# Kernel tuning notes

Measured on AMD Instinct MI355X. Metric: run time of the kernel, lower is better.

Reference implementation:

```python
import jax, jax.numpy as jnp
import numpy as np

N_NODES, N_EDGES = 16384, 8192
IN_CH, HID_CH = 256, 256
ALPHA, BETA = -1.5, -0.5


def setup_inputs() -> dict:
    key = jax.random.key(0)
    k1, k2, k3, k4, k5, k6 = jax.random.split(key, 6)
    x_0 = jax.random.normal(k1, (N_NODES, IN_CH), dtype=jnp.float32)
    # binary incidence matrix (n_nodes, n_edges)
    incidence_1 = jax.random.randint(k2, (N_NODES, N_EDGES), 0, 2).astype(jnp.float32)
    # conv weights (torch Conv: x @ W then neighborhood @ .)
    W0 = jax.random.normal(k3, (IN_CH, HID_CH), dtype=jnp.float32) * 0.02
    W1 = jax.random.normal(k4, (HID_CH, HID_CH), dtype=jnp.float32) * 0.02
    # xavier_uniform biases of shape (1, hidden)
    gain = 1.414
    bound = gain * np.sqrt(6.0 / (1 + HID_CH)) * np.sqrt(3.0) / np.sqrt(3.0)  # xavier bound = gain*sqrt(6/(fan_in+fan_out))
    bound = gain * np.sqrt(6.0 / (1 + HID_CH))
    bias_0_to_1 = jax.random.uniform(k5, (1, HID_CH), minval=-bound, maxval=bound, dtype=jnp.float32)
    bias_1_to_0 = jax.random.uniform(k6, (1, HID_CH), minval=-bound, maxval=bound, dtype=jnp.float32)
    return {"x_0": x_0, "incidence_1": incidence_1, "W0": W0, "W1": W1,
            "bias_0_to_1": bias_0_to_1, "bias_1_to_0": bias_1_to_0}


def _normalize_incidence(B1):
    # edge/node cardinalities raised to alpha/beta
    edge_card = jnp.sum(B1, axis=0) ** ALPHA          # (n_edges,)
    node_card = jnp.sum(B1, axis=1) ** BETA           # (n_nodes,)
    mask = (B1 > 0).astype(B1.dtype)
    d0_inv = 1.0 / (mask @ edge_card)                 # (n_nodes,) per-node sum of incident edge_card
    d1_inv = 1.0 / (mask.T @ node_card)               # (n_edges,) per-edge sum of member node_card
    # B1_norm = D0_left^-1 @ B1 @ diag(edge_card)
    B1_norm = d0_inv[:, None] * B1 * edge_card[None, :]
    # B1T_norm = D1_left^-1 @ B1^T @ diag(node_card)
    B1T_norm = d1_inv[:, None] * B1.T * node_card[None, :]
    return B1_norm, B1T_norm


def reference(x_0, incidence_1, W0, W1, bias_0_to_1, bias_1_to_0):
    B1_norm, B1T_norm = _normalize_incidence(incidence_1)
    # node -> edge conv: x_1 = B1T_norm @ (x_0 @ W0) + b01
    x_1 = B1T_norm @ (x_0 @ W0) + bias_0_to_1        # (n_edges, hid)
    # edge -> node conv: x_0 = B1_norm @ (x_1 @ W1) + b10
    x_0_out = B1_norm @ (x_1 @ W1) + bias_1_to_0     # (n_nodes, hid)
    return jax.nn.relu(x_0_out), jax.nn.relu(x_1)
```

## Files before the change

kernel.cpp:

```cpp
#include <hip/hip_runtime.h>
#include <stdint.h>

#define NN 16384
#define NE 8192
#define CH 256
#define MM1_SPLIT 8
#define MM2_SPLIT 4

typedef __attribute__((ext_vector_type(8))) short bf16x8;
typedef __attribute__((ext_vector_type(4))) float f32x4;

__device__ __forceinline__ unsigned short f2bf(float f) {
  unsigned u = __float_as_uint(f);
  u += 0x7FFFu + ((u >> 16) & 1u);
  return (unsigned short)(u >> 16);
}
__device__ __forceinline__ void async_copy16(const void* gptr, void* lptr) {
  __builtin_amdgcn_global_load_lds((const __attribute__((address_space(1))) unsigned int*)gptr,
                                   (__attribute__((address_space(3))) unsigned int*)lptr,
                                   16, 0, 0);
}

__device__ __forceinline__ void transpose32(unsigned* x) {
  const unsigned masks[5] = {0x0000FFFFu, 0x00FF00FFu, 0x0F0F0F0Fu, 0x33333333u, 0x55555555u};
#pragma unroll
  for (int jj = 0; jj < 5; ++jj) {
    const int j = 16 >> jj;
    const unsigned m = masks[jj];
#pragma unroll
    for (int k = 0; k < 32; ++k) {
      if ((k & j) == 0) {
        unsigned t = ((x[k] >> j) ^ x[k + j]) & m;
        x[k] ^= (t << j);
        x[k + j] ^= t;
      }
    }
  }
}

__global__ void k0_transpose_w(const float* __restrict__ W0, const float* __restrict__ W1,
                               unsigned short* __restrict__ W0T, unsigned short* __restrict__ W1T) {
  const float* W = blockIdx.y ? W1 : W0;
  unsigned short* WT = blockIdx.y ? W1T : W0T;
  int n = blockIdx.x;
  int k = threadIdx.x;
  WT[n * CH + k] = f2bf(W[k * CH + n]);
}

__global__ void k1_pack_card(const float* __restrict__ B1, unsigned* __restrict__ pk1,
                             float* __restrict__ node_card) {
  int n = blockIdx.x;
  int t = threadIdx.x;
  const float4* p = (const float4*)(B1 + (size_t)n * NE + t * 32);
  unsigned w = 0;
#pragma unroll
  for (int jj = 0; jj < 8; ++jj) {
    float4 v = p[jj];
    w |= ((__float_as_uint(v.x) >> 23) & 1u) << (4 * jj);
    w |= ((__float_as_uint(v.y) >> 23) & 1u) << (4 * jj + 1);
    w |= ((__float_as_uint(v.z) >> 23) & 1u) << (4 * jj + 2);
    w |= ((__float_as_uint(v.w) >> 23) & 1u) << (4 * jj + 3);
  }
  pk1[(size_t)n * 256 + t] = w;
  int s = __popc(w);
  __shared__ int red[4];
#pragma unroll
  for (int off = 32; off; off >>= 1) s += __shfl_down(s, off, 64);
  if ((t & 63) == 0) red[t >> 6] = s;
  __syncthreads();
  if (t == 0) {
    float tot = (float)(red[0] + red[1] + red[2] + red[3]);
    node_card[n] = rsqrtf(tot);
  }
}

__global__ __launch_bounds__(256) void k1b_bitT(const unsigned* __restrict__ pk1,
                                                unsigned* __restrict__ pk1T) {
  int bw = blockIdx.x & 127;
  int half = blockIdx.x >> 7;
  int t = threadIdx.x;
  int nt = half * 256 + t;
  unsigned x0[32], x1[32];
#pragma unroll
  for (int r = 0; r < 32; ++r) {
    uint2 v = *(const uint2*)&pk1[(size_t)(nt * 32 + r) * 256 + 2 * bw];
    x0[r] = v.x;
    x1[r] = v.y;
  }
  transpose32(x0);
  transpose32(x1);
  int e0 = bw * 64;
#pragma unroll
  for (int c = 0; c < 32; ++c) {
    pk1T[(size_t)(e0 + c) * 512 + nt] = x0[c];
    pk1T[(size_t)(e0 + 32 + c) * 512 + nt] = x1[c];
  }
}

__global__ __launch_bounds__(256) void k2_y0(const float* __restrict__ X0,
                                             const unsigned short* __restrict__ W0T,
                                             const float* __restrict__ node_card,
                                             unsigned short* __restrict__ y0sT) {
  __shared__ __align__(16) unsigned short a_lds[64 * 32];
  __shared__ __align__(16) unsigned short b_lds[256 * 32];
  const int tid = threadIdx.x;
  const int wave = tid >> 6, lane = tid & 63;
  const int quad = lane >> 4, l15 = lane & 15;
  const int m0 = blockIdx.x * 64;
  const int ar = tid >> 3, ac = (tid & 7) * 4;

  f32x4 acc[4][4];
  const f32x4 fz = {0.f, 0.f, 0.f, 0.f};
#pragma unroll
  for (int i = 0; i < 4; ++i)
#pragma unroll
    for (int j = 0; j < 4; ++j) acc[i][j] = fz;

  for (int k0 = 0; k0 < CH; k0 += 32) {
    __syncthreads();
#pragma unroll
    for (int p = 0; p < 2; ++p) {
      float4 v = *(const float4*)(X0 + (size_t)(m0 + ar + p * 32) * CH + k0 + ac);
      uint2 w;
      w.x = ((unsigned)f2bf(v.x)) | ((unsigned)f2bf(v.y) << 16);
      w.y = ((unsigned)f2bf(v.z)) | ((unsigned)f2bf(v.w) << 16);
      *(uint2*)&a_lds[(ar + p * 32) * 32 + ac] = w;
    }
#pragma unroll
    for (int i = 0; i < 4; ++i) {
      int rowbase = wave * 64 + i * 16;
      const unsigned short* g = W0T + (size_t)(rowbase + (lane >> 2)) * CH + k0 + (lane & 3) * 8;
      async_copy16(g, &b_lds[rowbase * 32]);
    }
    __syncthreads();
    bf16x8 af[4];
#pragma unroll
    for (int i = 0; i < 4; ++i)
      af[i] = *(const bf16x8*)&a_lds[(i * 16 + l15) * 32 + quad * 8];
#pragma unroll
    for (int j = 0; j < 4; ++j) {
      bf16x8 bfr = *(const bf16x8*)&b_lds[(wave * 64 + j * 16 + l15) * 32 + quad * 8];
#pragma unroll
      for (int i = 0; i < 4; ++i)
        acc[i][j] = __builtin_amdgcn_mfma_f32_16x16x32_bf16(af[i], bfr, acc[i][j], 0, 0, 0);
    }
  }
#pragma unroll
  for (int i = 0; i < 4; ++i) {
    int row4 = m0 + i * 16 + quad * 4;
    float4 nc = *(const float4*)(node_card + row4);
#pragma unroll
    for (int j = 0; j < 4; ++j) {
      int col = wave * 64 + j * 16 + l15;
      f32x4 v = acc[i][j];
      ushort4 o;
      o.x = f2bf(v[0] * nc.x);
      o.y = f2bf(v[1] * nc.y);
      o.z = f2bf(v[2] * nc.z);
      o.w = f2bf(v[3] * nc.w);
      *(ushort4*)&y0sT[(size_t)col * NN + row4] = o;
    }
  }
}

__global__ void k2b_aux(const float* __restrict__ node_card, unsigned short* __restrict__ y0sT) {
  int n = blockIdx.x * 256 + threadIdx.x;
  y0sT[(size_t)256 * NN + n] = f2bf(node_card[n]);
  y0sT[(size_t)257 * NN + n] = 0x3F80;
#pragma unroll
  for (int r = 258; r < 272; ++r) y0sT[(size_t)r * NN + n] = 0;
}

__global__ __launch_bounds__(256) void mm1_kernel(const unsigned char* __restrict__ pk1T,
                                                  const unsigned short* __restrict__ y0sT,
                                                  float* __restrict__ mm1p,
                                                  float* __restrict__ auxD,
                                                  float* __restrict__ auxC) {
  __shared__ __align__(16) unsigned short a_lds[64 * 40];
  __shared__ __align__(16) unsigned short b_lds[272 * 32];
  const int tid = threadIdx.x;
  const int wave = tid >> 6, lane = tid & 63;
  const int quad = lane >> 4, l15 = lane & 15;
  const int m0 = blockIdx.x * 64;
  const int sp = blockIdx.y;
  const int KS = NN / MM1_SPLIT;
  const int kbase = sp * KS;

  const int am = tid >> 2;
  const int akg = tid & 3;
  const int ajbs = akg ^ ((am >> 4) & 3);
  unsigned short* aw_dst = &a_lds[am * 40 + ajbs * 8];

  f32x4 acc[4][4];
  f32x4 acc5[4];
  const f32x4 fz = {0.f, 0.f, 0.f, 0.f};
#pragma unroll
  for (int i = 0; i < 4; ++i) {
    acc5[i] = fz;
#pragma unroll
    for (int j = 0; j < 4; ++j) acc[i][j] = fz;
  }

  const unsigned char* agp = pk1T + (size_t)(m0 + am) * (NN / 8) + (kbase >> 3) + akg;
  unsigned abyte = *agp;

  for (int kk = 0; kk < KS; kk += 32) {
    const int k0 = kbase + kk;
    __syncthreads();
    {
      uint4 aw;
#pragma unroll
      for (int j = 0; j < 4; ++j) {
        unsigned lo = (abyte >> (2 * j)) & 1u;
        unsigned hi = (abyte >> (2 * j + 1)) & 1u;
        ((unsigned*)&aw)[j] = lo * 0x3F80u + hi * 0x3F800000u;
      }
      *(uint4*)aw_dst = aw;
    }
#pragma unroll
    for (int i = 0; i < 4; ++i) {
      int rowbase = wave * 64 + i * 16;
      const unsigned short* g = y0sT + (size_t)(rowbase + (lane >> 2)) * NN + k0 + (lane & 3) * 8;
      async_copy16(g, &b_lds[rowbase * 32]);
    }
    if (wave == 3) {
      const unsigned short* g = y0sT + (size_t)(256 + (lane >> 2)) * NN + k0 + (lane & 3) * 8;
      async_copy16(g, &b_lds[256 * 32]);
    }
    __syncthreads();
    if (kk + 32 < KS) {
      agp += 4;
      abyte = *agp;
    }
    bf16x8 af[4];
#pragma unroll
    for (int i = 0; i < 4; ++i) {
      int m = i * 16 + l15;
      int jbs = quad ^ ((m >> 4) & 3);
      af[i] = *(const bf16x8*)&a_lds[m * 40 + jbs * 8];
    }
#pragma unroll
    for (int j = 0; j < 4; ++j) {
      bf16x8 bfr = *(const bf16x8*)&b_lds[(wave * 64 + j * 16 + l15) * 32 + quad * 8];
#pragma unroll
      for (int i = 0; i < 4; ++i)
        acc[i][j] = __builtin_amdgcn_mfma_f32_16x16x32_bf16(af[i], bfr, acc[i][j], 0, 0, 0);
    }
    if (wave == 3) {
      bf16x8 bfr = *(const bf16x8*)&b_lds[(256 + l15) * 32 + quad * 8];
#pragma unroll
      for (int i = 0; i < 4; ++i)
        acc5[i] = __builtin_amdgcn_mfma_f32_16x16x32_bf16(af[i], bfr, acc5[i], 0, 0, 0);
    }
  }
  float* outp = mm1p + (size_t)sp * NE * CH;
#pragma unroll
  for (int i = 0; i < 4; ++i) {
    int row4 = m0 + i * 16 + quad * 4;
#pragma unroll
    for (int j = 0; j < 4; ++j) {
      int col = wave * 64 + j * 16 + l15;
#pragma unroll
      for (int r = 0; r < 4; ++r) outp[(size_t)(row4 + r) * CH + col] = acc[i][j][r];
    }
  }
  if (wave == 3 && l15 < 2) {
    float* dst = (l15 == 0 ? auxD : auxC) + (size_t)sp * NE;
#pragma unroll
    for (int i = 0; i < 4; ++i) {
      int row4 = m0 + i * 16 + quad * 4;
#pragma unroll
      for (int r = 0; r < 4; ++r) dst[row4 + r] = acc5[i][r];
    }
  }
}

__global__ void k3_edge_final(const float* __restrict__ mm1p, const float* __restrict__ auxD,
                              const float* __restrict__ auxC, const float* __restrict__ b01,
                              float* __restrict__ out1, unsigned short* __restrict__ x1bf,
                              float* __restrict__ edge_card) {
  int e = blockIdx.x, c = threadIdx.x;
  float ds = 0.f, p = 0.f;
#pragma unroll
  for (int sp = 0; sp < MM1_SPLIT; ++sp) {
    ds += auxD[(size_t)sp * NE + e];
    p += mm1p[(size_t)sp * NE * CH + (size_t)e * CH + c];
  }
  float x1 = p / ds + b01[c];
  out1[(size_t)e * CH + c] = fmaxf(x1, 0.f);
  x1bf[(size_t)e * CH + c] = f2bf(x1);
  if (c == 0) {
    float cs = 0.f;
#pragma unroll
    for (int sp = 0; sp < MM1_SPLIT; ++sp) cs += auxC[(size_t)sp * NE + e];
    edge_card[e] = 1.0f / (cs * sqrtf(cs));
  }
}

__global__ __launch_bounds__(256) void k5_y1(const unsigned short* __restrict__ x1bf,
                                             const unsigned short* __restrict__ W1T,
                                             const float* __restrict__ edge_card,
                                             unsigned short* __restrict__ y1sT) {
  __shared__ __align__(16) unsigned short a_lds[64 * 32];
  __shared__ __align__(16) unsigned short b_lds[256 * 32];
  const int tid = threadIdx.x;
  const int wave = tid >> 6, lane = tid & 63;
  const int quad = lane >> 4, l15 = lane & 15;
  const int m0 = blockIdx.x * 64;

  f32x4 acc[4][4];
  const f32x4 fz = {0.f, 0.f, 0.f, 0.f};
#pragma unroll
  for (int i = 0; i < 4; ++i)
#pragma unroll
    for (int j = 0; j < 4; ++j) acc[i][j] = fz;

  for (int k0 = 0; k0 < CH; k0 += 32) {
    __syncthreads();
    {
      const unsigned short* g = x1bf + (size_t)(m0 + wave * 16 + (lane >> 2)) * CH + k0 + (lane & 3) * 8;
      async_copy16(g, &a_lds[(wave * 16) * 32]);
    }
#pragma unroll
    for (int i = 0; i < 4; ++i) {
      int rowbase = wave * 64 + i * 16;
      const unsigned short* g = W1T + (size_t)(rowbase + (lane >> 2)) * CH + k0 + (lane & 3) * 8;
      async_copy16(g, &b_lds[rowbase * 32]);
    }
    __syncthreads();
    bf16x8 af[4];
#pragma unroll
    for (int i = 0; i < 4; ++i)
      af[i] = *(const bf16x8*)&a_lds[(i * 16 + l15) * 32 + quad * 8];
#pragma unroll
    for (int j = 0; j < 4; ++j) {
      bf16x8 bfr = *(const bf16x8*)&b_lds[(wave * 64 + j * 16 + l15) * 32 + quad * 8];
#pragma unroll
      for (int i = 0; i < 4; ++i)
        acc[i][j] = __builtin_amdgcn_mfma_f32_16x16x32_bf16(af[i], bfr, acc[i][j], 0, 0, 0);
    }
  }
#pragma unroll
  for (int i = 0; i < 4; ++i) {
    int row4 = m0 + i * 16 + quad * 4;
    float4 ec = *(const float4*)(edge_card + row4);
#pragma unroll
    for (int j = 0; j < 4; ++j) {
      int col = wave * 64 + j * 16 + l15;
      f32x4 v = acc[i][j];
      ushort4 o;
      o.x = f2bf(v[0] * ec.x);
      o.y = f2bf(v[1] * ec.y);
      o.z = f2bf(v[2] * ec.z);
      o.w = f2bf(v[3] * ec.w);
      *(ushort4*)&y1sT[(size_t)col * NE + row4] = o;
    }
  }
}

__global__ void k5b_aux(const float* __restrict__ edge_card, unsigned short* __restrict__ y1sT) {
  int e = blockIdx.x * 256 + threadIdx.x;
  y1sT[(size_t)256 * NE + e] = f2bf(edge_card[e]);
#pragma unroll
  for (int r = 257; r < 272; ++r) y1sT[(size_t)r * NE + e] = 0;
}

__global__ __launch_bounds__(256) void mm2_kernel(const unsigned char* __restrict__ pk1,
                                                  const unsigned short* __restrict__ y1sT,
                                                  float* __restrict__ mm2p,
                                                  float* __restrict__ d0p) {
  __shared__ __align__(16) unsigned short a_lds[64 * 40];
  __shared__ __align__(16) unsigned short b_lds[272 * 32];
  const int tid = threadIdx.x;
  const int wave = tid >> 6, lane = tid & 63;
  const int quad = lane >> 4, l15 = lane & 15;
  const int m0 = blockIdx.x * 64;
  const int sp = blockIdx.y;
  const int KS = NE / MM2_SPLIT;
  const int kbase = sp * KS;

  const int am = tid >> 2;
  const int akg = tid & 3;
  unsigned short* aw_dst = &a_lds[am * 40 + akg * 8];

  f32x4 acc[4][4];
  f32x4 acc5[4];
  const f32x4 fz = {0.f, 0.f, 0.f, 0.f};
#pragma unroll
  for (int i = 0; i < 4; ++i) {
    acc5[i] = fz;
#pragma unroll
    for (int j = 0; j < 4; ++j) acc[i][j] = fz;
  }

  const unsigned char* agp = pk1 + (size_t)(m0 + am) * (NE / 8) + (kbase >> 3) + akg;
  unsigned abyte = *agp;

  for (int kk = 0; kk < KS; kk += 32) {
    const int k0 = kbase + kk;
    __syncthreads();
    {
      uint4 aw;
#pragma unroll
      for (int j = 0; j < 4; ++j) {
        unsigned lo = (abyte >> (2 * j)) & 1u;
        unsigned hi = (abyte >> (2 * j + 1)) & 1u;
        ((unsigned*)&aw)[j] = lo * 0x3F80u + hi * 0x3F800000u;
      }
      *(uint4*)aw_dst = aw;
    }
#pragma unroll
    for (int i = 0; i < 4; ++i) {
      int rowbase = wave * 64 + i * 16;
      const unsigned short* g = y1sT + (size_t)(rowbase + (lane >> 2)) * NE + k0 + (lane & 3) * 8;
      async_copy16(g, &b_lds[rowbase * 32]);
    }
    if (wave == 3) {
      const unsigned short* g = y1sT + (size_t)(256 + (lane >> 2)) * NE + k0 + (lane & 3) * 8;
      async_copy16(g, &b_lds[256 * 32]);
    }
    __syncthreads();
    if (kk + 32 < KS) {
      agp += 4;
      abyte = *agp;
    }
    bf16x8 af[4];
#pragma unroll
    for (int i = 0; i < 4; ++i)
      af[i] = *(const bf16x8*)&a_lds[(i * 16 + l15) * 40 + quad * 8];
#pragma unroll
    for (int j = 0; j < 4; ++j) {
      bf16x8 bfr = *(const bf16x8*)&b_lds[(wave * 64 + j * 16 + l15) * 32 + quad * 8];
#pragma unroll
      for (int i = 0; i < 4; ++i)
        acc[i][j] = __builtin_amdgcn_mfma_f32_16x16x32_bf16(af[i], bfr, acc[i][j], 0, 0, 0);
    }
    if (wave == 3) {
      bf16x8 bfr = *(const bf16x8*)&b_lds[(256 + l15) * 32 + quad * 8];
#pragma unroll
      for (int i = 0; i < 4; ++i)
        acc5[i] = __builtin_amdgcn_mfma_f32_16x16x32_bf16(af[i], bfr, acc5[i], 0, 0, 0);
    }
  }
  float* outp = mm2p + (size_t)sp * NN * CH;
#pragma unroll
  for (int i = 0; i < 4; ++i) {
    int row4 = m0 + i * 16 + quad * 4;
#pragma unroll
    for (int j = 0; j < 4; ++j) {
      int col = wave * 64 + j * 16 + l15;
#pragma unroll
      for (int r = 0; r < 4; ++r) outp[(size_t)(row4 + r) * CH + col] = acc[i][j][r];
    }
  }
  if (wave == 3 && l15 == 0) {
#pragma unroll
    for (int i = 0; i < 4; ++i) {
      int row4 = m0 + i * 16 + quad * 4;
#pragma unroll
      for (int r = 0; r < 4; ++r) d0p[(size_t)sp * NN + row4 + r] = acc5[i][r];
    }
  }
}

__global__ void k6_node_final(const float* __restrict__ mm2p, const float* __restrict__ d0p,
                              const float* __restrict__ b10, float* __restrict__ out0) {
  int n = blockIdx.x, c = threadIdx.x;
  float s = 0.f, d = 0.f;
#pragma unroll
  for (int sp = 0; sp < MM2_SPLIT; ++sp) {
    s += mm2p[(size_t)sp * NN * CH + (size_t)n * CH + c];
    d += d0p[(size_t)sp * NN + n];
  }
  float v = s / d + b10[c];
  out0[(size_t)n * CH + c] = fmaxf(v, 0.f);
}

extern "C" void kernel_launch(void* const* d_in, const int* in_sizes, int n_in,
                              void* d_out, int out_size, void* d_ws, size_t ws_size,
                              hipStream_t stream) {
  const float* x0 = (const float*)d_in[0];
  const float* B1 = (const float*)d_in[1];
  const float* W0 = (const float*)d_in[2];
  const float* W1 = (const float*)d_in[3];
  const float* b01 = (const float*)d_in[4];
  const float* b10 = (const float*)d_in[5];
  float* out0 = (float*)d_out;
  float* out1 = out0 + (size_t)NN * CH;

  char* ws = (char*)d_ws;
  size_t off = 0;
  auto take = [&](size_t bytes) {
    void* p = ws + off;
    off += (bytes + 255) & ~(size_t)255;
    return p;
  };
  unsigned short* y0sT = (unsigned short*)take((size_t)272 * NN * 2);
  unsigned short* y1sT = (unsigned short*)take((size_t)272 * NE * 2);
  unsigned short* x1bf = (unsigned short*)take((size_t)NE * CH * 2);
  float* mm1p = (float*)take((size_t)MM1_SPLIT * NE * CH * 4);
  float* mm2p = mm1p;
  float* node_card = (float*)take((size_t)NN * 4);
  float* edge_card = (float*)take((size_t)NE * 4);
  float* auxD = (float*)take((size_t)MM1_SPLIT * NE * 4);
  float* auxC = (float*)take((size_t)MM1_SPLIT * NE * 4);
  float* d0p = (float*)take((size_t)MM2_SPLIT * NN * 4);
  unsigned short* W0T = (unsigned short*)take((size_t)CH * CH * 2);
  unsigned short* W1T = (unsigned short*)take((size_t)CH * CH * 2);
  unsigned* pk1 = (unsigned*)take((size_t)NN * 256 * 4);
  unsigned* pk1T = (unsigned*)take((size_t)NE * 512 * 4);
  (void)ws_size; (void)in_sizes; (void)n_in; (void)out_size;

  k0_transpose_w<<<dim3(256, 2), 256, 0, stream>>>(W0, W1, W0T, W1T);
  k1_pack_card<<<NN, 256, 0, stream>>>(B1, pk1, node_card);
  k1b_bitT<<<256, 256, 0, stream>>>(pk1, pk1T);
  k2_y0<<<NN / 64, 256, 0, stream>>>(x0, W0T, node_card, y0sT);
  k2b_aux<<<NN / 256, 256, 0, stream>>>(node_card, y0sT);
  mm1_kernel<<<dim3(NE / 64, MM1_SPLIT), 256, 0, stream>>>((const unsigned char*)pk1T, y0sT, mm1p, auxD, auxC);
  k3_edge_final<<<NE, 256, 0, stream>>>(mm1p, auxD, auxC, b01, out1, x1bf, edge_card);
  k5_y1<<<NE / 64, 256, 0, stream>>>(x1bf, W1T, edge_card, y1sT);
  k5b_aux<<<NE / 256, 256, 0, stream>>>(edge_card, y1sT);
  mm2_kernel<<<dim3(NN / 64, MM2_SPLIT), 256, 0, stream>>>((const unsigned char*)pk1, y1sT, mm2p, d0p);
  k6_node_final<<<NN, 256, 0, stream>>>(mm2p, d0p, b10, out0);
}
```

Measured before the change: 1.085 ms.

## Enlarge mm tiles to 128x256 with 8 waves and compute degree sums on CUDA cores

```diff
diff --git a/kernel.cpp b/kernel.cpp
--- a/kernel.cpp
+++ b/kernel.cpp
@@ -94,6 +94,21 @@
   for (int c = 0; c < 32; ++c) {
     pk1T[(size_t)(e0 + c) * 512 + nt] = x0[c];
     pk1T[(size_t)(e0 + 32 + c) * 512 + nt] = x1[c];
+  }
+}
+
+__global__ void kcs_edge_card(const unsigned* __restrict__ pk1T, float* __restrict__ edge_card) {
+  int lane = threadIdx.x & 63;
+  int e = blockIdx.x * 4 + (threadIdx.x >> 6);
+  const uint4* p = (const uint4*)(pk1T + (size_t)e * 512) + lane * 2;
+  uint4 a = p[0], b = p[1];
+  int s = __popc(a.x) + __popc(a.y) + __popc(a.z) + __popc(a.w) +
+          __popc(b.x) + __popc(b.y) + __popc(b.z) + __popc(b.w);
+#pragma unroll
+  for (int off = 32; off; off >>= 1) s += __shfl_down(s, off, 64);
+  if (lane == 0) {
+    float cs = (float)s;
+    edge_card[e] = 1.0f / (cs * sqrtf(cs));
   }
 }
 
@@ -166,23 +181,23 @@
 __global__ void k2b_aux(const float* __restrict__ node_card, unsigned short* __restrict__ y0sT) {
   int n = blockIdx.x * 256 + threadIdx.x;
   y0sT[(size_t)256 * NN + n] = f2bf(node_card[n]);
-  y0sT[(size_t)257 * NN + n] = 0x3F80;
-#pragma unroll
-  for (int r = 258; r < 272; ++r) y0sT[(size_t)r * NN + n] = 0;
-}
-
-__global__ __launch_bounds__(256) void mm1_kernel(const unsigned char* __restrict__ pk1T,
-                                                  const unsigned short* __restrict__ y0sT,
-                                                  float* __restrict__ mm1p,
-                                                  float* __restrict__ auxD,
-                                                  float* __restrict__ auxC) {
-  __shared__ __align__(16) unsigned short a_lds[64 * 40];
+#pragma unroll
+  for (int r = 257; r < 272; ++r) y0sT[(size_t)r * NN + n] = 0;
+}
+
+__global__ __launch_bounds__(512, 4) void mm1_kernel(const unsigned char* __restrict__ pk1T,
+                                                     const unsigned short* __restrict__ y0sT,
+                                                     float* __restrict__ mm1p,
+                                                     float* __restrict__ auxD) {
+  __shared__ __align__(16) unsigned short a_lds[128 * 40];
   __shared__ __align__(16) unsigned short b_lds[272 * 32];
   const int tid = threadIdx.x;
   const int wave = tid >> 6, lane = tid & 63;
   const int quad = lane >> 4, l15 = lane & 15;
-  const int m0 = blockIdx.x * 64;
-  const int sp = blockIdx.y;
+  const int wm = wave >> 2, wn = wave & 3;
+  const int bid = blockIdx.x;
+  const int sp = bid & 7;
+  const int m0 = (bid >> 3) * 128;
   const int KS = NN / MM1_SPLIT;
   const int kbase = sp * KS;
 
@@ -192,38 +207,37 @@
   unsigned short* aw_dst = &a_lds[am * 40 + ajbs * 8];
 
   f32x4 acc[4][4];
-  f32x4 acc5[4];
   const f32x4 fz = {0.f, 0.f, 0.f, 0.f};
 #pragma unroll
-  for (int i = 0; i < 4; ++i) {
-    acc5[i] = fz;
+  for (int i = 0; i < 4; ++i)
 #pragma unroll
     for (int j = 0; j < 4; ++j) acc[i][j] = fz;
-  }
+  float daux = 0.f;
 
   const unsigned char* agp = pk1T + (size_t)(m0 + am) * (NN / 8) + (kbase >> 3) + akg;
   unsigned abyte = *agp;
 
   for (int kk = 0; kk < KS; kk += 32) {
     const int k0 = kbase + kk;
+    const unsigned abcur = abyte;
     __syncthreads();
     {
       uint4 aw;
 #pragma unroll
       for (int j = 0; j < 4; ++j) {
-        unsigned lo = (abyte >> (2 * j)) & 1u;
-        unsigned hi = (abyte >> (2 * j + 1)) & 1u;
+        unsigned lo = (abcur >> (2 * j)) & 1u;
+        unsigned hi = (abcur >> (2 * j + 1)) & 1u;
         ((unsigned*)&aw)[j] = lo * 0x3F80u + hi * 0x3F800000u;
       }
       *(uint4*)aw_dst = aw;
     }
 #pragma unroll
-    for (int i = 0; i < 4; ++i) {
-      int rowbase = wave * 64 + i * 16;
+    for (int i = 0; i < 2; ++i) {
+      int rowbase = wave * 32 + i * 16;
       const unsigned short* g = y0sT + (size_t)(rowbase + (lane >> 2)) * NN + k0 + (lane & 3) * 8;
       async_copy16(g, &b_lds[rowbase * 32]);
     }
-    if (wave == 3) {
+    if (wave == 7) {
       const unsigned short* g = y0sT + (size_t)(256 + (lane >> 2)) * NN + k0 + (lane & 3) * 8;
       async_copy16(g, &b_lds[256 * 32]);
     }
@@ -232,53 +246,55 @@
       agp += 4;
       abyte = *agp;
     }
+    {
+      bf16x8 nc8 = *(const bf16x8*)&b_lds[256 * 32 + akg * 8];
+      float part = 0.f;
+#pragma unroll
+      for (int j = 0; j < 8; ++j) {
+        float ncf = __uint_as_float(((unsigned)(unsigned short)nc8[j]) << 16);
+        part += ((abcur >> j) & 1u) ? ncf : 0.f;
+      }
+      daux += part;
+    }
     bf16x8 af[4];
 #pragma unroll
     for (int i = 0; i < 4; ++i) {
-      int m = i * 16 + l15;
-      int jbs = quad ^ ((m >> 4) & 3);
+      int m = wm * 64 + i * 16 + l15;
+      int jbs = quad ^ i;
       af[i] = *(const bf16x8*)&a_lds[m * 40 + jbs * 8];
     }
 #pragma unroll
     for (int j = 0; j < 4; ++j) {
-      bf16x8 bfr = *(const bf16x8*)&b_lds[(wave * 64 + j * 16 + l15) * 32 + quad * 8];
+      bf16x8 bfr = *(const bf16x8*)&b_lds[(wn * 64 + j * 16 + l15) * 32 + quad * 8];
 #pragma unroll
       for (int i = 0; i < 4; ++i)
         acc[i][j] = __builtin_amdgcn_mfma_f32_16x16x32_bf16(af[i], bfr, acc[i][j], 0, 0, 0);
     }
-    if (wave == 3) {
-      bf16x8 bfr = *(const bf16x8*)&b_lds[(256 + l15) * 32 + quad * 8];
-#pragma unroll
-      for (int i = 0; i < 4; ++i)
-        acc5[i] = __builtin_amdgcn_mfma_f32_16x16x32_bf16(af[i], bfr, acc5[i], 0, 0, 0);
-    }
   }
   float* outp = mm1p + (size_t)sp * NE * CH;
 #pragma unroll
   for (int i = 0; i < 4; ++i) {
-    int row4 = m0 + i * 16 + quad * 4;
-#pragma unroll
-    for (int j = 0; j < 4; ++j) {
-      int col = wave * 64 + j * 16 + l15;
+    int row4 = m0 + wm * 64 + i * 16 + quad * 4;
+#pragma unroll
+    for (int j = 0; j < 4; ++j) {
+      int col = wn * 64 + j * 16 + l15;
 #pragma unroll
       for (int r = 0; r < 4; ++r) outp[(size_t)(row4 + r) * CH + col] = acc[i][j][r];
     }
   }
-  if (wave == 3 && l15 < 2) {
-    float* dst = (l15 == 0 ? auxD : auxC) + (size_t)sp * NE;
-#pragma unroll
-    for (int i = 0; i < 4; ++i) {
-      int row4 = m0 + i * 16 + quad * 4;
-#pragma unroll
-      for (int r = 0; r < 4; ++r) dst[row4 + r] = acc5[i][r];
-    }
+  __syncthreads();
+  float* dred = (float*)a_lds;
+  dred[tid] = daux;
+  __syncthreads();
+  if (tid < 128) {
+    float s = dred[tid * 4] + dred[tid * 4 + 1] + dred[tid * 4 + 2] + dred[tid * 4 + 3];
+    auxD[(size_t)sp * NE + m0 + tid] = s;
   }
 }
 
 __global__ void k3_edge_final(const float* __restrict__ mm1p, const float* __restrict__ auxD,
-                              const float* __restrict__ auxC, const float* __restrict__ b01,
-                              float* __restrict__ out1, unsigned short* __restrict__ x1bf,
-                              float* __restrict__ edge_card) {
+                              const float* __restrict__ b01,
+                              float* __restrict__ out1, unsigned short* __restrict__ x1bf) {
   int e = blockIdx.x, c = threadIdx.x;
   float ds = 0.f, p = 0.f;
 #pragma unroll
@@ -289,12 +305,6 @@
   float x1 = p / ds + b01[c];
   out1[(size_t)e * CH + c] = fmaxf(x1, 0.f);
   x1bf[(size_t)e * CH + c] = f2bf(x1);
-  if (c == 0) {
-    float cs = 0.f;
-#pragma unroll
-    for (int sp = 0; sp < MM1_SPLIT; ++sp) cs += auxC[(size_t)sp * NE + e];
-    edge_card[e] = 1.0f / (cs * sqrtf(cs));
-  }
 }
 
 __global__ __launch_bounds__(256) void k5_y1(const unsigned short* __restrict__ x1bf,
@@ -365,57 +375,59 @@
   for (int r = 257; r < 272; ++r) y1sT[(size_t)r * NE + e] = 0;
 }
 
-__global__ __launch_bounds__(256) void mm2_kernel(const unsigned char* __restrict__ pk1,
-                                                  const unsigned short* __restrict__ y1sT,
-                                                  float* __restrict__ mm2p,
-                                                  float* __restrict__ d0p) {
-  __shared__ __align__(16) unsigned short a_lds[64 * 40];
+__global__ __launch_bounds__(512, 4) void mm2_kernel(const unsigned char* __restrict__ pk1,
+                                                     const unsigned short* __restrict__ y1sT,
+                                                     float* __restrict__ mm2p,
+                                                     float* __restrict__ d0p) {
+  __shared__ __align__(16) unsigned short a_lds[128 * 40];
   __shared__ __align__(16) unsigned short b_lds[272 * 32];
   const int tid = threadIdx.x;
   const int wave = tid >> 6, lane = tid & 63;
   const int quad = lane >> 4, l15 = lane & 15;
-  const int m0 = blockIdx.x * 64;
-  const int sp = blockIdx.y;
+  const int wm = wave >> 2, wn = wave & 3;
+  const int bid = blockIdx.x;
+  const int sp = (bid >> 1) & 3;
+  const int m0 = (((bid >> 3) << 1) | (bid & 1)) * 128;
   const int KS = NE / MM2_SPLIT;
   const int kbase = sp * KS;
 
   const int am = tid >> 2;
   const int akg = tid & 3;
-  unsigned short* aw_dst = &a_lds[am * 40 + akg * 8];
+  const int ajbs = akg ^ ((am >> 4) & 3);
+  unsigned short* aw_dst = &a_lds[am * 40 + ajbs * 8];
 
   f32x4 acc[4][4];
-  f32x4 acc5[4];
   const f32x4 fz = {0.f, 0.f, 0.f, 0.f};
 #pragma unroll
-  for (int i = 0; i < 4; ++i) {
-    acc5[i] = fz;
+  for (int i = 0; i < 4; ++i)
 #pragma unroll
     for (int j = 0; j < 4; ++j) acc[i][j] = fz;
-  }
+  float daux = 0.f;
 
   const unsigned char* agp = pk1 + (size_t)(m0 + am) * (NE / 8) + (kbase >> 3) + akg;
   unsigned abyte = *agp;
 
   for (int kk = 0; kk < KS; kk += 32) {
     const int k0 = kbase + kk;
+    const unsigned abcur = abyte;
     __syncthreads();
     {
       uint4 aw;
 #pragma unroll
       for (int j = 0; j < 4; ++j) {
-        unsigned lo = (abyte >> (2 * j)) & 1u;
-        unsigned hi = (abyte >> (2 * j + 1)) & 1u;
+        unsigned lo = (abcur >> (2 * j)) & 1u;
+        unsigned hi = (abcur >> (2 * j + 1)) & 1u;
         ((unsigned*)&aw)[j] = lo * 0x3F80u + hi * 0x3F800000u;
       }
       *(uint4*)aw_dst = aw;
     }
 #pragma unroll
-    for (int i = 0; i < 4; ++i) {
-      int rowbase = wave * 64 + i * 16;
+    for (int i = 0; i < 2; ++i) {
+      int rowbase = wave * 32 + i * 16;
       const unsigned short* g = y1sT + (size_t)(rowbase + (lane >> 2)) * NE + k0 + (lane & 3) * 8;
       async_copy16(g, &b_lds[rowbase * 32]);
     }
-    if (wave == 3) {
+    if (wave == 7) {
       const unsigned short* g = y1sT + (size_t)(256 + (lane >> 2)) * NE + k0 + (lane & 3) * 8;
       async_copy16(g, &b_lds[256 * 32]);
     }
@@ -424,42 +436,49 @@
       agp += 4;
       abyte = *agp;
     }
+    {
+      bf16x8 ec8 = *(const bf16x8*)&b_lds[256 * 32 + akg * 8];
+      float part = 0.f;
+#pragma unroll
+      for (int j = 0; j < 8; ++j) {
+        float ecf = __uint_as_float(((unsigned)(unsigned short)ec8[j]) << 16);
+        part += ((abcur >> j) & 1u) ? ecf : 0.f;
+      }
+      daux += part;
+    }
     bf16x8 af[4];
 #pragma unroll
-    for (int i = 0; i < 4; ++i)
-      af[i] = *(const bf16x8*)&a_lds[(i * 16 + l15) * 40 + quad * 8];
-#pragma unroll
-    for (int j = 0; j < 4; ++j) {
-      bf16x8 bfr = *(const bf16x8*)&b_lds[(wave * 64 + j * 16 + l15) * 32 + quad * 8];
+    for (int i = 0; i < 4; ++i) {
+      int m = wm * 64 + i * 16 + l15;
+      int jbs = quad ^ i;
+      af[i] = *(const bf16x8*)&a_lds[m * 40 + jbs * 8];
+    }
+#pragma unroll
+    for (int j = 0; j < 4; ++j) {
+      bf16x8 bfr = *(const bf16x8*)&b_lds[(wn * 64 + j * 16 + l15) * 32 + quad * 8];
 #pragma unroll
       for (int i = 0; i < 4; ++i)
         acc[i][j] = __builtin_amdgcn_mfma_f32_16x16x32_bf16(af[i], bfr, acc[i][j], 0, 0, 0);
     }
-    if (wave == 3) {
-      bf16x8 bfr = *(const bf16x8*)&b_lds[(256 + l15) * 32 + quad * 8];
-#pragma unroll
-      for (int i = 0; i < 4; ++i)
-        acc5[i] = __builtin_amdgcn_mfma_f32_16x16x32_bf16(af[i], bfr, acc5[i], 0, 0, 0);
-    }
   }
   float* outp = mm2p + (size_t)sp * NN * CH;
 #pragma unroll
   for (int i = 0; i < 4; ++i) {
-    int row4 = m0 + i * 16 + quad * 4;
-#pragma unroll
-    for (int j = 0; j < 4; ++j) {
-      int col = wave * 64 + j * 16 + l15;
+    int row4 = m0 + wm * 64 + i * 16 + quad * 4;
+#pragma unroll
+    for (int j = 0; j < 4; ++j) {
+      int col = wn * 64 + j * 16 + l15;
 #pragma unroll
       for (int r = 0; r < 4; ++r) outp[(size_t)(row4 + r) * CH + col] = acc[i][j][r];
     }
   }
-  if (wave == 3 && l15 == 0) {
-#pragma unroll
-    for (int i = 0; i < 4; ++i) {
-      int row4 = m0 + i * 16 + quad * 4;
-#pragma unroll
-      for (int r = 0; r < 4; ++r) d0p[(size_t)sp * NN + row4 + r] = acc5[i][r];
-    }
+  __syncthreads();
+  float* dred = (float*)a_lds;
+  dred[tid] = daux;
+  __syncthreads();
+  if (tid < 128) {
+    float s = dred[tid * 4] + dred[tid * 4 + 1] + dred[tid * 4 + 2] + dred[tid * 4 + 3];
+    d0p[(size_t)sp * NN + m0 + tid] = s;
   }
 }
 
@@ -503,7 +522,6 @@
   float* node_card = (float*)take((size_t)NN * 4);
   float* edge_card = (float*)take((size_t)NE * 4);
   float* auxD = (float*)take((size_t)MM1_SPLIT * NE * 4);
-  float* auxC = (float*)take((size_t)MM1_SPLIT * NE * 4);
   float* d0p = (float*)take((size_t)MM2_SPLIT * NN * 4);
   unsigned short* W0T = (unsigned short*)take((size_t)CH * CH * 2);
   unsigned short* W1T = (unsigned short*)take((size_t)CH * CH * 2);
@@ -514,12 +532,13 @@
   k0_transpose_w<<<dim3(256, 2), 256, 0, stream>>>(W0, W1, W0T, W1T);
   k1_pack_card<<<NN, 256, 0, stream>>>(B1, pk1, node_card);
   k1b_bitT<<<256, 256, 0, stream>>>(pk1, pk1T);
+  kcs_edge_card<<<NE / 4, 256, 0, stream>>>(pk1T, edge_card);
   k2_y0<<<NN / 64, 256, 0, stream>>>(x0, W0T, node_card, y0sT);
   k2b_aux<<<NN / 256, 256, 0, stream>>>(node_card, y0sT);
-  mm1_kernel<<<dim3(NE / 64, MM1_SPLIT), 256, 0, stream>>>((const unsigned char*)pk1T, y0sT, mm1p, auxD, auxC);
-  k3_edge_final<<<NE, 256, 0, stream>>>(mm1p, auxD, auxC, b01, out1, x1bf, edge_card);
+  mm1_kernel<<<512, 512, 0, stream>>>((const unsigned char*)pk1T, y0sT, mm1p, auxD);
+  k3_edge_final<<<NE, 256, 0, stream>>>(mm1p, auxD, b01, out1, x1bf);
   k5_y1<<<NE / 64, 256, 0, stream>>>(x1bf, W1T, edge_card, y1sT);
   k5b_aux<<<NE / 256, 256, 0, stream>>>(edge_card, y1sT);
-  mm2_kernel<<<dim3(NN / 64, MM2_SPLIT), 256, 0, stream>>>((const unsigned char*)pk1, y1sT, mm2p, d0p);
+  mm2_kernel<<<512, 512, 0, stream>>>((const unsigned char*)pk1, y1sT, mm2p, d0p);
   k6_node_final<<<NN, 256, 0, stream>>>(mm2p, d0p, b10, out0);
 }
```

After: 977.2 us. -10.0%, faster.
